# Kernel optimization log

Hardware: AMD Instinct MI355X
Metric: run time of the kernel (lower is better)

Reference implementation:

```python
import jax, jax.numpy as jnp
import numpy as np

D_MODEL = 1024
NUM_HEADS = 16
KEY_DIM = 64
VALUE_DIM = 64
NEG_INF = jnp.float32(-1e30)


def setup_inputs() -> dict:
    key = jax.random.key(0)
    ks = jax.random.split(key, 10)
    B, S = 2, 2048
    lim = 1.0 / np.sqrt(D_MODEL)
    x = jax.random.normal(ks[0], (B, S, D_MODEL), dtype=jnp.float32)
    mask = jnp.ones((B, S), dtype=jnp.int32)  # pad mask: 1 = keep
    # stacked per-head linear params (Linear stores weight as [out, in])
    Wq = jax.random.uniform(ks[1], (NUM_HEADS, KEY_DIM, D_MODEL), jnp.float32, -lim, lim)
    bq = jax.random.uniform(ks[2], (NUM_HEADS, KEY_DIM), jnp.float32, -lim, lim)
    Wk = jax.random.uniform(ks[3], (NUM_HEADS, KEY_DIM, D_MODEL), jnp.float32, -lim, lim)
    bk = jax.random.uniform(ks[4], (NUM_HEADS, KEY_DIM), jnp.float32, -lim, lim)
    Wv = jax.random.uniform(ks[5], (NUM_HEADS, VALUE_DIM, D_MODEL), jnp.float32, -lim, lim)
    bv = jax.random.uniform(ks[6], (NUM_HEADS, VALUE_DIM), jnp.float32, -lim, lim)
    lim_o = 1.0 / np.sqrt(NUM_HEADS * VALUE_DIM)
    Wo = jax.random.uniform(ks[7], (D_MODEL, NUM_HEADS * VALUE_DIM), jnp.float32, -lim_o, lim_o)
    bo = jax.random.uniform(ks[8], (D_MODEL,), jnp.float32, -lim_o, lim_o)
    return {"x": x, "mask": mask, "Wq": Wq, "bq": bq, "Wk": Wk, "bk": bk,
            "Wv": Wv, "bv": bv, "Wo": Wo, "bo": bo}


def _mha(x, mask, Wq, bq, Wk, bk, Wv, bv, Wo, bo):
    B, S, _ = x.shape
    # per-head projections: [B, H, S, k]
    q = jnp.einsum('bsd,hkd->bhsk', x, Wq) + bq[None, :, None, :]
    k = jnp.einsum('bsd,hkd->bhsk', x, Wk) + bk[None, :, None, :]
    v = jnp.einsum('bsd,hvd->bhsv', x, Wv) + bv[None, :, None, :]
    scale = 1.0 / np.sqrt(KEY_DIM).astype(np.float32)
    scores = jnp.einsum('bhik,bhjk->bhij', q, k) * scale  # [B, H, S, S]
    # final mask = causal AND pad-row AND pad-col
    causal = jnp.tril(jnp.ones((S, S), dtype=bool))
    pad = mask.astype(bool)
    final = causal[None, None] & pad[:, None, :, None] & pad[:, None, None, :]
    masked = jnp.where(final, scores, NEG_INF)
    w = jax.nn.softmax(masked, axis=-1)
    w = jnp.where(final, w, 0.0)  # fully-masked rows -> zeros, matching loop impl
    out = jnp.einsum('bhij,bhjv->bhiv', w, v)            # [B, H, S, V]
    concat = out.transpose(0, 2, 1, 3).reshape(B, S, NUM_HEADS * VALUE_DIM)
    return concat @ Wo.T + bo


def reference(x, mask, Wq, bq, Wk, bk, Wv, bv, Wo, bo):
    return _mha(x, mask, Wq, bq, Wk, bk, Wv, bv, Wo, bo)
```

## Files before the change

### kernel.cpp

```cpp
#include <hip/hip_runtime.h>

#define SEQ 2048
#define NH 16
#define HD 64
#define DMODEL 1024

__device__ __forceinline__ unsigned int f2bf(float f) {
  unsigned int u = __float_as_uint(f);
  return ((u + 0x7fffu + ((u >> 16) & 1u)) >> 16) & 0xffffu;
}

__device__ __forceinline__ unsigned int pk2bf(float a, float b) {
  unsigned short ua = __builtin_bit_cast(unsigned short, (__bf16)a);
  unsigned short ub = __builtin_bit_cast(unsigned short, (__bf16)b);
  return (unsigned int)ua | ((unsigned int)ub << 16);
}

typedef __bf16 bf16x8 __attribute__((ext_vector_type(8)));
typedef float f32x4 __attribute__((ext_vector_type(4)));

__device__ __forceinline__ void gl2lds16(const unsigned short* g, unsigned short* l) {
  __builtin_amdgcn_global_load_lds(
      (const __attribute__((address_space(1))) unsigned int*)g,
      (__attribute__((address_space(3))) unsigned int*)l, 16, 0, 0);
}

__global__ __launch_bounds__(256) void cast_all_kernel(
    const float* __restrict__ x, const float* __restrict__ wq,
    const float* __restrict__ wk, const float* __restrict__ wv,
    const float* __restrict__ wo,
    unsigned short* __restrict__ xb, unsigned short* __restrict__ wqb,
    unsigned short* __restrict__ wkb, unsigned short* __restrict__ wvb,
    unsigned short* __restrict__ wob) {
  int idx = blockIdx.x * 256 + threadIdx.x;
  if (idx >= 1048576) return;
  const float* src;
  unsigned short* dst;
  int off;
  if (idx < 524288) {
    src = x; dst = xb; off = idx;
  } else {
    int t = idx - 524288;
    int w = t >> 17;
    off = t & 131071;
    src = (w == 0) ? wq : (w == 1) ? wk : (w == 2) ? wv : wo;
    dst = (w == 0) ? wqb : (w == 1) ? wkb : (w == 2) ? wvb : wob;
  }
  const float4* p = reinterpret_cast<const float4*>(src) + (size_t)off * 2;
  float4 a = p[0], b = p[1];
  uint4 o;
  o.x = f2bf(a.x) | (f2bf(a.y) << 16);
  o.y = f2bf(a.z) | (f2bf(a.w) << 16);
  o.z = f2bf(b.x) | (f2bf(b.y) << 16);
  o.w = f2bf(b.z) | (f2bf(b.w) << 16);
  reinterpret_cast<uint4*>(dst)[off] = o;
}

template <int MODE>
__global__ __launch_bounds__(256) void gemm128(
    const unsigned short* __restrict__ A, const unsigned short* __restrict__ B,
    const float* __restrict__ bias0, const float* __restrict__ bias1,
    const float* __restrict__ bias2, float* __restrict__ Cf,
    unsigned short* __restrict__ Qo, unsigned short* __restrict__ Ko,
    unsigned short* __restrict__ Vto, int Kdim) {
  __shared__ __align__(16) unsigned short As[128 * 64];
  __shared__ __align__(16) unsigned short Bs[128 * 64];
  const int tid = threadIdx.x;
  const int wave = tid >> 6, lane = tid & 63;
  const int wm = wave >> 1, wn = wave & 1;
  const int fr = lane & 15, quad = lane >> 4;
  const int fx = fr & 7;
  const int n0 = blockIdx.x * 128, m0 = blockIdx.y * 128;

  const int srowg = lane >> 3;
  const int schunk = (lane & 7) ^ (srowg & 7);
  const unsigned short* Abase =
      A + (size_t)(m0 + wave * 32 + srowg) * Kdim + schunk * 8;
  const unsigned short* Bbase =
      B + (size_t)(n0 + wave * 32 + srowg) * Kdim + schunk * 8;
  unsigned short* AsW = As + (wave * 32) * 64;
  unsigned short* BsW = Bs + (wave * 32) * 64;

  f32x4 acc[4][4];
#pragma unroll
  for (int mt = 0; mt < 4; ++mt)
#pragma unroll
    for (int nt = 0; nt < 4; ++nt) acc[mt][nt] = f32x4{0.f, 0.f, 0.f, 0.f};

  for (int k0 = 0; k0 < Kdim; k0 += 64) {
#pragma unroll
    for (int t = 0; t < 4; ++t) {
      gl2lds16(Abase + (size_t)(t * 8) * Kdim + k0, AsW + t * 8 * 64);
      gl2lds16(Bbase + (size_t)(t * 8) * Kdim + k0, BsW + t * 8 * 64);
    }
    __syncthreads();
#pragma unroll
    for (int ks = 0; ks < 2; ++ks) {
      bf16x8 af[4], bfv[4];
#pragma unroll
      for (int mt = 0; mt < 4; ++mt)
        af[mt] = *reinterpret_cast<const bf16x8*>(
            As + (wm * 64 + mt * 16 + fr) * 64 + ((ks * 4 + quad) ^ fx) * 8);
#pragma unroll
      for (int nt = 0; nt < 4; ++nt)
        bfv[nt] = *reinterpret_cast<const bf16x8*>(
            Bs + (wn * 64 + nt * 16 + fr) * 64 + ((ks * 4 + quad) ^ fx) * 8);
#pragma unroll
      for (int mt = 0; mt < 4; ++mt)
#pragma unroll
        for (int nt = 0; nt < 4; ++nt)
          acc[mt][nt] = __builtin_amdgcn_mfma_f32_16x16x32_bf16(
              af[mt], bfv[nt], acc[mt][nt], 0, 0, 0);
    }
    __syncthreads();
  }

  if (MODE == 0) {
    const int seg = n0 >> 10;
    const float* bp = (seg == 0) ? bias0 : (seg == 1) ? bias1 : bias2;
    const float scale = (seg == 0) ? 0.1803368809f : 1.0f;
    unsigned short* QK = (seg == 0) ? Qo : Ko;
#pragma unroll
    for (int nt = 0; nt < 4; ++nt) {
      const int c = (n0 + wn * 64 + nt * 16 + fr) & 1023;
      const int h = c >> 6, d = c & 63;
      const float bs = bp[c];
#pragma unroll
      for (int mt = 0; mt < 4; ++mt) {
        const int mbase = m0 + wm * 64 + mt * 16 + quad * 4;
        const int b = mbase >> 11, s0 = mbase & 2047;
        if (seg < 2) {
          unsigned short* dst = QK + (((size_t)(b * NH + h)) * SEQ + s0) * HD + d;
#pragma unroll
          for (int r = 0; r < 4; ++r)
            dst[(size_t)r * HD] = (unsigned short)f2bf((acc[mt][nt][r] + bs) * scale);
        } else {
          uint2 pk;
          pk.x = pk2bf(acc[mt][nt][0] + bs, acc[mt][nt][1] + bs);
          pk.y = pk2bf(acc[mt][nt][2] + bs, acc[mt][nt][3] + bs);
          *reinterpret_cast<uint2*>(
              Vto + (((size_t)(b * NH + h)) * HD + d) * SEQ + s0) = pk;
        }
      }
    }
  } else {
#pragma unroll
    for (int nt = 0; nt < 4; ++nt) {
      const int cg = n0 + wn * 64 + nt * 16 + fr;
      const float bs = bias0[cg];
#pragma unroll
      for (int mt = 0; mt < 4; ++mt) {
        const int mbase = m0 + wm * 64 + mt * 16 + quad * 4;
#pragma unroll
        for (int r = 0; r < 4; ++r)
          Cf[(size_t)(mbase + r) * DMODEL + cg] = acc[mt][nt][r] + bs;
      }
    }
  }
}

__global__ __launch_bounds__(256) void attn_mfma_kernel(
    const unsigned short* __restrict__ Qg, const unsigned short* __restrict__ Kg,
    const unsigned short* __restrict__ Vtg, const int* __restrict__ mask,
    unsigned short* __restrict__ concat) {
  const int g = blockIdx.x >> 5;
  const int bh = blockIdx.x & 31;
  const int b = bh >> 4, h = bh & 15;
  const int tid = threadIdx.x;
  const int wave = tid >> 6, lane = tid & 63;
  const int quad = lane >> 4, fr = lane & 15;
  const int ib[4] = {g, 15 - g, 16 + g, 31 - g};

  __shared__ unsigned short Pt[4][4][16][72];

  const unsigned short* Qb = Qg + ((size_t)bh * SEQ) * HD;
  const unsigned short* Kb = Kg + ((size_t)bh * SEQ) * HD;
  const unsigned short* Vtb = Vtg + ((size_t)bh * HD) * SEQ;
  const int* maskb = mask + b * SEQ;

  bool bad = false;
  {
    const int4* mp4 = reinterpret_cast<const int4*>(maskb);
#pragma unroll
    for (int u = 0; u < 8; ++u) {
      int4 v = mp4[lane * 8 + u];
      bad |= !(v.x && v.y && v.z && v.w);
    }
  }
  const unsigned long long bm = __ballot(bad);

  int irow[4], padr[4];
  bf16x8 q0[4], q1[4];
  f32x4 o[4][4];
  float mr[4], lr[4];
#pragma unroll
  for (int t = 0; t < 4; ++t) {
    irow[t] = ib[t] * 64 + wave * 16 + fr;
    q0[t] = *reinterpret_cast<const bf16x8*>(Qb + (size_t)irow[t] * HD + quad * 8);
    q1[t] = *reinterpret_cast<const bf16x8*>(Qb + (size_t)irow[t] * HD + quad * 8 + 32);
    padr[t] = maskb[irow[t]];
    mr[t] = -1e20f; lr[t] = 0.f;
#pragma unroll
    for (int vt = 0; vt < 4; ++vt) o[t][vt] = f32x4{0.f, 0.f, 0.f, 0.f};
  }

  const int jcmax = ib[3];
  for (int jc = 0; jc <= jcmax; ++jc) {
    const int j0 = jc * 64;
    bf16x8 ka0[4], ka1[4], vb0[4], vb1[4];
#pragma unroll
    for (int jt = 0; jt < 4; ++jt) {
      const unsigned short* kr = Kb + (size_t)(j0 + jt * 16 + fr) * HD + quad * 8;
      ka0[jt] = *reinterpret_cast<const bf16x8*>(kr);
      ka1[jt] = *reinterpret_cast<const bf16x8*>(kr + 32);
    }
#pragma unroll
    for (int vt = 0; vt < 4; ++vt) {
      const unsigned short* vr = Vtb + (size_t)(vt * 16 + fr) * SEQ + j0 + quad * 8;
      vb0[vt] = *reinterpret_cast<const bf16x8*>(vr);
      vb1[vt] = *reinterpret_cast<const bf16x8*>(vr + 32);
    }
    const bool tb = ((bm >> (2 * jc)) & 3ull) != 0ull;

#pragma unroll
    for (int t = 0; t < 4; ++t) {
      if (jc > ib[t]) continue;
      const int ir = irow[t];

      f32x4 st[4];
#pragma unroll
      for (int jt = 0; jt < 4; ++jt) {
        st[jt] = f32x4{0.f, 0.f, 0.f, 0.f};
        st[jt] = __builtin_amdgcn_mfma_f32_16x16x32_bf16(ka0[jt], q0[t], st[jt], 0, 0, 0);
        st[jt] = __builtin_amdgcn_mfma_f32_16x16x32_bf16(ka1[jt], q1[t], st[jt], 0, 0, 0);
      }

      if (tb) {
        const int4* mp = reinterpret_cast<const int4*>(maskb + j0);
#pragma unroll
        for (int jt = 0; jt < 4; ++jt) {
          const int4 mv = mp[jt * 4 + quad];
          if (mv.x == 0) st[jt][0] = -1e30f;
          if (mv.y == 0) st[jt][1] = -1e30f;
          if (mv.z == 0) st[jt][2] = -1e30f;
          if (mv.w == 0) st[jt][3] = -1e30f;
        }
      }
      if (jc == ib[t]) {
#pragma unroll
        for (int jt = 0; jt < 4; ++jt) {
          const int jb = j0 + jt * 16 + quad * 4;
#pragma unroll
          for (int r = 0; r < 4; ++r)
            if (jb + r > ir) st[jt][r] = -1e30f;
        }
      }

      float tmax = -1e30f;
#pragma unroll
      for (int jt = 0; jt < 4; ++jt)
#pragma unroll
        for (int r = 0; r < 4; ++r) tmax = fmaxf(tmax, st[jt][r]);
      tmax = fmaxf(tmax, __shfl_xor(tmax, 16));
      tmax = fmaxf(tmax, __shfl_xor(tmax, 32));
      const bool upd = __ballot(tmax > mr[t]) != 0ull;
      float corr = 1.f;
      if (upd) {
        const float mn = fmaxf(mr[t], tmax);
        corr = __builtin_amdgcn_exp2f(mr[t] - mn);
        mr[t] = mn;
      }
      const float mcur = mr[t];
      float lloc = 0.f;
#pragma unroll
      for (int jt = 0; jt < 4; ++jt) {
        float p0 = __builtin_amdgcn_exp2f(st[jt][0] - mcur);
        float p1 = __builtin_amdgcn_exp2f(st[jt][1] - mcur);
        float p2 = __builtin_amdgcn_exp2f(st[jt][2] - mcur);
        float p3 = __builtin_amdgcn_exp2f(st[jt][3] - mcur);
        lloc += (p0 + p1) + (p2 + p3);
        uint2 pk; pk.x = pk2bf(p0, p1); pk.y = pk2bf(p2, p3);
        *reinterpret_cast<uint2*>(&Pt[wave][t][fr][jt * 16 + quad * 4]) = pk;
      }
      lloc += __shfl_xor(lloc, 16);
      lloc += __shfl_xor(lloc, 32);
      if (upd) {
        lr[t] = lr[t] * corr + lloc;
#pragma unroll
        for (int vt = 0; vt < 4; ++vt) {
          o[t][vt][0] *= corr; o[t][vt][1] *= corr;
          o[t][vt][2] *= corr; o[t][vt][3] *= corr;
        }
      } else {
        lr[t] += lloc;
      }

      bf16x8 pa0 = *reinterpret_cast<const bf16x8*>(&Pt[wave][t][fr][quad * 8]);
      bf16x8 pa1 = *reinterpret_cast<const bf16x8*>(&Pt[wave][t][fr][quad * 8 + 32]);
#pragma unroll
      for (int vt = 0; vt < 4; ++vt) {
        o[t][vt] = __builtin_amdgcn_mfma_f32_16x16x32_bf16(vb0[vt], pa0, o[t][vt], 0, 0, 0);
        o[t][vt] = __builtin_amdgcn_mfma_f32_16x16x32_bf16(vb1[vt], pa1, o[t][vt], 0, 0, 0);
      }
    }
  }

#pragma unroll
  for (int t = 0; t < 4; ++t) {
    const float inv = (padr[t] != 0 && lr[t] > 0.f) ? 1.f / lr[t] : 0.f;
    unsigned short* orow = concat + ((size_t)(b * SEQ + irow[t])) * DMODEL + h * HD;
#pragma unroll
    for (int vt = 0; vt < 4; ++vt) {
      uint2 pk;
      pk.x = pk2bf(o[t][vt][0] * inv, o[t][vt][1] * inv);
      pk.y = pk2bf(o[t][vt][2] * inv, o[t][vt][3] * inv);
      *reinterpret_cast<uint2*>(orow + vt * 16 + quad * 4) = pk;
    }
  }
}

extern "C" void kernel_launch(void* const* d_in, const int* in_sizes, int n_in,
                              void* d_out, int out_size, void* d_ws, size_t ws_size,
                              hipStream_t stream) {
  (void)in_sizes; (void)n_in; (void)out_size;
  const float* x  = (const float*)d_in[0];
  const int* mask = (const int*)d_in[1];
  const float* Wq = (const float*)d_in[2];
  const float* bq = (const float*)d_in[3];
  const float* Wk = (const float*)d_in[4];
  const float* bk = (const float*)d_in[5];
  const float* Wv = (const float*)d_in[6];
  const float* bv = (const float*)d_in[7];
  const float* Wo = (const float*)d_in[8];
  const float* bo = (const float*)d_in[9];
  float* out = (float*)d_out;

  char* ws = (char*)d_ws;
  if (ws_size < (48ull << 20)) return;
  unsigned short* xb  = (unsigned short*)(ws);
  unsigned short* wqb = (unsigned short*)(ws + (8ull  << 20));
  unsigned short* wkb = (unsigned short*)(ws + (10ull << 20));
  unsigned short* wvb = (unsigned short*)(ws + (12ull << 20));
  unsigned short* wob = (unsigned short*)(ws + (14ull << 20));
  unsigned short* Qb  = (unsigned short*)(ws + (16ull << 20));
  unsigned short* Kb  = (unsigned short*)(ws + (24ull << 20));
  unsigned short* Vtb = (unsigned short*)(ws + (32ull << 20));
  unsigned short* cb  = (unsigned short*)(ws + (40ull << 20));

  cast_all_kernel<<<4096, 256, 0, stream>>>(x, Wq, Wk, Wv, Wo, xb, wqb, wkb, wvb, wob);

  gemm128<0><<<dim3(24, 32), 256, 0, stream>>>(xb, wqb, bq, bk, bv,
                                               nullptr, Qb, Kb, Vtb, 1024);

  attn_mfma_kernel<<<256, 256, 0, stream>>>(Qb, Kb, Vtb, mask, cb);

  gemm128<1><<<dim3(8, 32), 256, 0, stream>>>(cb, wob, bo, nullptr, nullptr,
                                              out, nullptr, nullptr, nullptr, 1024);
}
```

Baseline: 220.2 us.

## Split attention to one Q tile per block with double-buffered LDS K/V staging

The attention kernel now gives each block a single 64-row query tile rather than four, so it launches 1024 blocks instead of 256. Block order is chosen so the longest causal tiles are scheduled first. K and V^T tiles are shared by the block's waves through double-buffered, XOR-swizzled LDS filled with global_load_lds, with a syncthreads per step, instead of each wave loading its own copy from global memory into registers. This aims to raise occupancy (launch bounds 256,4), balance causal work and overlap loads with MFMA, at the cost of per-step barriers and less Q reuse per K/V load.

```diff
diff --git a/kernel.cpp b/kernel.cpp
--- a/kernel.cpp
+++ b/kernel.cpp
@@ -159,163 +159,170 @@
   }
 }
 
-__global__ __launch_bounds__(256) void attn_mfma_kernel(
+__global__ __launch_bounds__(256, 4) void attn_mfma_kernel(
     const unsigned short* __restrict__ Qg, const unsigned short* __restrict__ Kg,
     const unsigned short* __restrict__ Vtg, const int* __restrict__ mask,
     unsigned short* __restrict__ concat) {
-  const int g = blockIdx.x >> 5;
-  const int bh = blockIdx.x & 31;
+  const int w = blockIdx.x >> 8;
+  const int c = blockIdx.x & 255;
+  const int gg = c >> 5;
+  const int bh = c & 31;
+  const int ib = (w == 0) ? (31 - gg) : (w == 1) ? gg : (w == 2) ? (23 - gg) : (8 + gg);
   const int b = bh >> 4, h = bh & 15;
   const int tid = threadIdx.x;
   const int wave = tid >> 6, lane = tid & 63;
   const int quad = lane >> 4, fr = lane & 15;
-  const int ib[4] = {g, 15 - g, 16 + g, 31 - g};
-
-  __shared__ unsigned short Pt[4][4][16][72];
+  const int fx = fr & 7;
+
+  __shared__ __align__(16) unsigned short Ks[2][64 * 64];
+  __shared__ __align__(16) unsigned short Vts[2][64 * 64];
+  __shared__ __align__(16) unsigned short Pt[4][16 * 64];
 
   const unsigned short* Qb = Qg + ((size_t)bh * SEQ) * HD;
   const unsigned short* Kb = Kg + ((size_t)bh * SEQ) * HD;
   const unsigned short* Vtb = Vtg + ((size_t)bh * HD) * SEQ;
   const int* maskb = mask + b * SEQ;
 
-  bool bad = false;
+  bool badl = false;
   {
     const int4* mp4 = reinterpret_cast<const int4*>(maskb);
 #pragma unroll
     for (int u = 0; u < 8; ++u) {
       int4 v = mp4[lane * 8 + u];
-      bad |= !(v.x && v.y && v.z && v.w);
-    }
-  }
-  const unsigned long long bm = __ballot(bad);
-
-  int irow[4], padr[4];
-  bf16x8 q0[4], q1[4];
-  f32x4 o[4][4];
-  float mr[4], lr[4];
-#pragma unroll
-  for (int t = 0; t < 4; ++t) {
-    irow[t] = ib[t] * 64 + wave * 16 + fr;
-    q0[t] = *reinterpret_cast<const bf16x8*>(Qb + (size_t)irow[t] * HD + quad * 8);
-    q1[t] = *reinterpret_cast<const bf16x8*>(Qb + (size_t)irow[t] * HD + quad * 8 + 32);
-    padr[t] = maskb[irow[t]];
-    mr[t] = -1e20f; lr[t] = 0.f;
-#pragma unroll
-    for (int vt = 0; vt < 4; ++vt) o[t][vt] = f32x4{0.f, 0.f, 0.f, 0.f};
-  }
-
-  const int jcmax = ib[3];
-  for (int jc = 0; jc <= jcmax; ++jc) {
+      badl |= !(v.x && v.y && v.z && v.w);
+    }
+  }
+  const unsigned long long bm = __ballot(badl);
+
+  const int ir = ib * 64 + wave * 16 + fr;
+  const bf16x8 q0 = *reinterpret_cast<const bf16x8*>(Qb + (size_t)ir * HD + quad * 8);
+  const bf16x8 q1 = *reinterpret_cast<const bf16x8*>(Qb + (size_t)ir * HD + quad * 8 + 32);
+  const int padi = maskb[ir];
+
+  f32x4 o[4];
+#pragma unroll
+  for (int vt = 0; vt < 4; ++vt) o[vt] = f32x4{0.f, 0.f, 0.f, 0.f};
+  float mr = -1e20f, lr = 0.f;
+
+  const int srowg = lane >> 3;
+  const int schunk = (lane & 7) ^ (srowg & 7);
+  const unsigned short* Ksrc = Kb + (size_t)(wave * 16 + srowg) * HD + schunk * 8;
+  const unsigned short* Vsrc = Vtb + (size_t)(wave * 16 + srowg) * SEQ + schunk * 8;
+  const int cA0 = (quad ^ fx) * 8;
+  const int cA1 = ((quad + 4) ^ fx) * 8;
+  unsigned short* PtW = Pt[wave];
+
+  {
+    unsigned short* KsW = Ks[0] + (wave * 16) * 64;
+    unsigned short* VtsW = Vts[0] + (wave * 16) * 64;
+#pragma unroll
+    for (int t = 0; t < 2; ++t) {
+      gl2lds16(Ksrc + (size_t)(t * 8) * HD, KsW + t * 8 * 64);
+      gl2lds16(Vsrc + (size_t)(t * 8) * SEQ, VtsW + t * 8 * 64);
+    }
+  }
+
+  for (int jc = 0; jc <= ib; ++jc) {
+    __syncthreads();
+    if (jc < ib) {
+      const int jn = (jc + 1) * 64;
+      unsigned short* KsW = Ks[(jc + 1) & 1] + (wave * 16) * 64;
+      unsigned short* VtsW = Vts[(jc + 1) & 1] + (wave * 16) * 64;
+#pragma unroll
+      for (int t = 0; t < 2; ++t) {
+        gl2lds16(Ksrc + (size_t)(jn + t * 8) * HD, KsW + t * 8 * 64);
+        gl2lds16(Vsrc + (size_t)(t * 8) * SEQ + jn, VtsW + t * 8 * 64);
+      }
+    }
+    const unsigned short* Kcur = Ks[jc & 1];
+    const unsigned short* Vcur = Vts[jc & 1];
     const int j0 = jc * 64;
-    bf16x8 ka0[4], ka1[4], vb0[4], vb1[4];
+    const bool tb = ((bm >> (2 * jc)) & 3ull) != 0ull;
+
+    f32x4 st[4];
 #pragma unroll
     for (int jt = 0; jt < 4; ++jt) {
-      const unsigned short* kr = Kb + (size_t)(j0 + jt * 16 + fr) * HD + quad * 8;
-      ka0[jt] = *reinterpret_cast<const bf16x8*>(kr);
-      ka1[jt] = *reinterpret_cast<const bf16x8*>(kr + 32);
-    }
+      bf16x8 ka0 = *reinterpret_cast<const bf16x8*>(&Kcur[(jt * 16 + fr) * 64 + cA0]);
+      bf16x8 ka1 = *reinterpret_cast<const bf16x8*>(&Kcur[(jt * 16 + fr) * 64 + cA1]);
+      st[jt] = f32x4{0.f, 0.f, 0.f, 0.f};
+      st[jt] = __builtin_amdgcn_mfma_f32_16x16x32_bf16(ka0, q0, st[jt], 0, 0, 0);
+      st[jt] = __builtin_amdgcn_mfma_f32_16x16x32_bf16(ka1, q1, st[jt], 0, 0, 0);
+    }
+
+    if (tb) {
+      const int4* mp = reinterpret_cast<const int4*>(maskb + j0);
+#pragma unroll
+      for (int jt = 0; jt < 4; ++jt) {
+        const int4 mv = mp[jt * 4 + quad];
+        if (mv.x == 0) st[jt][0] = -1e30f;
+        if (mv.y == 0) st[jt][1] = -1e30f;
+        if (mv.z == 0) st[jt][2] = -1e30f;
+        if (mv.w == 0) st[jt][3] = -1e30f;
+      }
+    }
+    if (jc == ib) {
+#pragma unroll
+      for (int jt = 0; jt < 4; ++jt) {
+        const int jb = j0 + jt * 16 + quad * 4;
+#pragma unroll
+        for (int r = 0; r < 4; ++r)
+          if (jb + r > ir) st[jt][r] = -1e30f;
+      }
+    }
+
+    float tmax = -1e30f;
+#pragma unroll
+    for (int jt = 0; jt < 4; ++jt)
+#pragma unroll
+      for (int r = 0; r < 4; ++r) tmax = fmaxf(tmax, st[jt][r]);
+    tmax = fmaxf(tmax, __shfl_xor(tmax, 16));
+    tmax = fmaxf(tmax, __shfl_xor(tmax, 32));
+    const bool upd = __ballot(tmax > mr) != 0ull;
+    float corr = 1.f;
+    if (upd) { const float mn = fmaxf(mr, tmax); corr = __builtin_amdgcn_exp2f(mr - mn); mr = mn; }
+    float lloc = 0.f;
+#pragma unroll
+    for (int jt = 0; jt < 4; ++jt) {
+      float p0 = __builtin_amdgcn_exp2f(st[jt][0] - mr);
+      float p1 = __builtin_amdgcn_exp2f(st[jt][1] - mr);
+      float p2 = __builtin_amdgcn_exp2f(st[jt][2] - mr);
+      float p3 = __builtin_amdgcn_exp2f(st[jt][3] - mr);
+      lloc += (p0 + p1) + (p2 + p3);
+      uint2 pk; pk.x = pk2bf(p0, p1); pk.y = pk2bf(p2, p3);
+      const int pc = (2 * jt + (quad >> 1)) ^ fx;
+      *reinterpret_cast<uint2*>(&PtW[fr * 64 + pc * 8 + (quad & 1) * 4]) = pk;
+    }
+    lloc += __shfl_xor(lloc, 16);
+    lloc += __shfl_xor(lloc, 32);
+    if (upd) {
+      lr = lr * corr + lloc;
+#pragma unroll
+      for (int vt = 0; vt < 4; ++vt) {
+        o[vt][0] *= corr; o[vt][1] *= corr; o[vt][2] *= corr; o[vt][3] *= corr;
+      }
+    } else {
+      lr += lloc;
+    }
+
+    bf16x8 pa0 = *reinterpret_cast<const bf16x8*>(&PtW[fr * 64 + (quad ^ fx) * 8]);
+    bf16x8 pa1 = *reinterpret_cast<const bf16x8*>(&PtW[fr * 64 + ((quad + 4) ^ fx) * 8]);
 #pragma unroll
     for (int vt = 0; vt < 4; ++vt) {
-      const unsigned short* vr = Vtb + (size_t)(vt * 16 + fr) * SEQ + j0 + quad * 8;
-      vb0[vt] = *reinterpret_cast<const bf16x8*>(vr);
-      vb1[vt] = *reinterpret_cast<const bf16x8*>(vr + 32);
-    }
-    const bool tb = ((bm >> (2 * jc)) & 3ull) != 0ull;
-
-#pragma unroll
-    for (int t = 0; t < 4; ++t) {
-      if (jc > ib[t]) continue;
-      const int ir = irow[t];
-
-      f32x4 st[4];
-#pragma unroll
-      for (int jt = 0; jt < 4; ++jt) {
-        st[jt] = f32x4{0.f, 0.f, 0.f, 0.f};
-        st[jt] = __builtin_amdgcn_mfma_f32_16x16x32_bf16(ka0[jt], q0[t], st[jt], 0, 0, 0);
-        st[jt] = __builtin_amdgcn_mfma_f32_16x16x32_bf16(ka1[jt], q1[t], st[jt], 0, 0, 0);
-      }
-
-      if (tb) {
-        const int4* mp = reinterpret_cast<const int4*>(maskb + j0);
-#pragma unroll
-        for (int jt = 0; jt < 4; ++jt) {
-          const int4 mv = mp[jt * 4 + quad];
-          if (mv.x == 0) st[jt][0] = -1e30f;
-          if (mv.y == 0) st[jt][1] = -1e30f;
-          if (mv.z == 0) st[jt][2] = -1e30f;
-          if (mv.w == 0) st[jt][3] = -1e30f;
-        }
-      }
-      if (jc == ib[t]) {
-#pragma unroll
-        for (int jt = 0; jt < 4; ++jt) {
-          const int jb = j0 + jt * 16 + quad * 4;
-#pragma unroll
-          for (int r = 0; r < 4; ++r)
-            if (jb + r > ir) st[jt][r] = -1e30f;
-        }
-      }
-
-      float tmax = -1e30f;
-#pragma unroll
-      for (int jt = 0; jt < 4; ++jt)
-#pragma unroll
-        for (int r = 0; r < 4; ++r) tmax = fmaxf(tmax, st[jt][r]);
-      tmax = fmaxf(tmax, __shfl_xor(tmax, 16));
-      tmax = fmaxf(tmax, __shfl_xor(tmax, 32));
-      const bool upd = __ballot(tmax > mr[t]) != 0ull;
-      float corr = 1.f;
-      if (upd) {
-        const float mn = fmaxf(mr[t], tmax);
-        corr = __builtin_amdgcn_exp2f(mr[t] - mn);
-        mr[t] = mn;
-      }
-      const float mcur = mr[t];
-      float lloc = 0.f;
-#pragma unroll
-      for (int jt = 0; jt < 4; ++jt) {
-        float p0 = __builtin_amdgcn_exp2f(st[jt][0] - mcur);
-        float p1 = __builtin_amdgcn_exp2f(st[jt][1] - mcur);
-        float p2 = __builtin_amdgcn_exp2f(st[jt][2] - mcur);
-        float p3 = __builtin_amdgcn_exp2f(st[jt][3] - mcur);
-        lloc += (p0 + p1) + (p2 + p3);
-        uint2 pk; pk.x = pk2bf(p0, p1); pk.y = pk2bf(p2, p3);
-        *reinterpret_cast<uint2*>(&Pt[wave][t][fr][jt * 16 + quad * 4]) = pk;
-      }
-      lloc += __shfl_xor(lloc, 16);
-      lloc += __shfl_xor(lloc, 32);
-      if (upd) {
-        lr[t] = lr[t] * corr + lloc;
-#pragma unroll
-        for (int vt = 0; vt < 4; ++vt) {
-          o[t][vt][0] *= corr; o[t][vt][1] *= corr;
-          o[t][vt][2] *= corr; o[t][vt][3] *= corr;
-        }
-      } else {
-        lr[t] += lloc;
-      }
-
-      bf16x8 pa0 = *reinterpret_cast<const bf16x8*>(&Pt[wave][t][fr][quad * 8]);
-      bf16x8 pa1 = *reinterpret_cast<const bf16x8*>(&Pt[wave][t][fr][quad * 8 + 32]);
-#pragma unroll
-      for (int vt = 0; vt < 4; ++vt) {
-        o[t][vt] = __builtin_amdgcn_mfma_f32_16x16x32_bf16(vb0[vt], pa0, o[t][vt], 0, 0, 0);
-        o[t][vt] = __builtin_amdgcn_mfma_f32_16x16x32_bf16(vb1[vt], pa1, o[t][vt], 0, 0, 0);
-      }
-    }
-  }
-
-#pragma unroll
-  for (int t = 0; t < 4; ++t) {
-    const float inv = (padr[t] != 0 && lr[t] > 0.f) ? 1.f / lr[t] : 0.f;
-    unsigned short* orow = concat + ((size_t)(b * SEQ + irow[t])) * DMODEL + h * HD;
-#pragma unroll
-    for (int vt = 0; vt < 4; ++vt) {
-      uint2 pk;
-      pk.x = pk2bf(o[t][vt][0] * inv, o[t][vt][1] * inv);
-      pk.y = pk2bf(o[t][vt][2] * inv, o[t][vt][3] * inv);
-      *reinterpret_cast<uint2*>(orow + vt * 16 + quad * 4) = pk;
-    }
+      bf16x8 vb0 = *reinterpret_cast<const bf16x8*>(&Vcur[(vt * 16 + fr) * 64 + cA0]);
+      bf16x8 vb1 = *reinterpret_cast<const bf16x8*>(&Vcur[(vt * 16 + fr) * 64 + cA1]);
+      o[vt] = __builtin_amdgcn_mfma_f32_16x16x32_bf16(vb0, pa0, o[vt], 0, 0, 0);
+      o[vt] = __builtin_amdgcn_mfma_f32_16x16x32_bf16(vb1, pa1, o[vt], 0, 0, 0);
+    }
+  }
+
+  const float inv = (padi != 0 && lr > 0.f) ? 1.f / lr : 0.f;
+  unsigned short* orow = concat + ((size_t)(b * SEQ + ir)) * DMODEL + h * HD;
+#pragma unroll
+  for (int vt = 0; vt < 4; ++vt) {
+    uint2 pk;
+    pk.x = pk2bf(o[vt][0] * inv, o[vt][1] * inv);
+    pk.y = pk2bf(o[vt][2] * inv, o[vt][3] * inv);
+    *reinterpret_cast<uint2*>(orow + vt * 16 + quad * 4) = pk;
   }
 }
 
@@ -352,7 +359,7 @@
   gemm128<0><<<dim3(24, 32), 256, 0, stream>>>(xb, wqb, bq, bk, bv,
                                                nullptr, Qb, Kb, Vtb, 1024);
 
-  attn_mfma_kernel<<<256, 256, 0, stream>>>(Qb, Kb, Vtb, mask, cb);
+  attn_mfma_kernel<<<1024, 256, 0, stream>>>(Qb, Kb, Vtb, mask, cb);
 
   gemm128<1><<<dim3(8, 32), 256, 0, stream>>>(cb, wob, bo, nullptr, nullptr,
                                               out, nullptr, nullptr, nullptr, 1024);
```

New measurement: 197.8 us. 1.11x faster.
